# Optimization experiments

Hardware: AMD Instinct MI355X
Metric: run time of the kernel (lower is better)

The kernel has to match this reference:

```python
import jax, jax.numpy as jnp
import numpy as np

BETA = 0.25
LATENT_DIM = 256
CODEBOOK_DIM = 2048
CODE_DIM = 64


def setup_inputs() -> dict:
    key = jax.random.key(0)
    k_z, k_wi, k_bi, k_cb, k_wo, k_bo = jax.random.split(key, 6)
    z = jax.random.normal(k_z, (64, LATENT_DIM, 32, 32), dtype=jnp.float32)
    # project_in: Conv2d(latent_dim, code_dim, kernel_size=1) -> weight [code_dim, latent_dim]
    W_in = jax.random.normal(k_wi, (CODE_DIM, LATENT_DIM), dtype=jnp.float32) * (1.0 / np.sqrt(LATENT_DIM))
    b_in = jax.random.normal(k_bi, (CODE_DIM,), dtype=jnp.float32) * 0.01
    # codebook init: uniform(-1/codebook_dim, 1/codebook_dim) as in _codebook_init
    codebook = jax.random.uniform(k_cb, (CODEBOOK_DIM, CODE_DIM), dtype=jnp.float32,
                                  minval=-1.0 / CODEBOOK_DIM, maxval=1.0 / CODEBOOK_DIM)
    # project_out: Conv2d(code_dim, latent_dim, kernel_size=1) -> weight [latent_dim, code_dim]
    W_out = jax.random.normal(k_wo, (LATENT_DIM, CODE_DIM), dtype=jnp.float32) * (1.0 / np.sqrt(CODE_DIM))
    b_out = jax.random.normal(k_bo, (LATENT_DIM,), dtype=jnp.float32) * 0.01
    return {"z": z, "W_in": W_in, "b_in": b_in, "codebook": codebook, "W_out": W_out, "b_out": b_out}


def reference(z, W_in, b_in, codebook, W_out, b_out):
    sg = jax.lax.stop_gradient
    # project_in: 1x1 conv == per-pixel linear
    zp = jnp.einsum('bchw,dc->bdhw', z, W_in) + b_in[None, :, None, None]  # [b, code_dim, h, w]
    b, c, h, w = zp.shape
    ze = zp.transpose(0, 2, 3, 1).reshape(-1, c)  # [(b h w), code_dim]
    # euclidean distances: ||z||^2 - 2 z.W^T + ||W||^2
    dist = (jnp.sum(ze * ze, axis=1, keepdims=True)
            - 2.0 * ze @ codebook.T
            + jnp.sum(codebook * codebook, axis=1))  # [(b h w), codebook_dim]
    idx = jnp.argmin(dist, axis=1)  # [(b h w)]
    # decoder: embedding lookup
    zq = codebook[idx].reshape(b, h, w, c).transpose(0, 3, 1, 2)  # [b, code_dim, h, w]
    # VQ loss: codebook loss + beta * commitment loss
    codebook_loss = jnp.mean((zq - sg(zp)) ** 2)
    embedding_loss = jnp.mean((sg(zq) - zp) ** 2)
    loss = codebook_loss + BETA * embedding_loss
    # straight-through estimator
    zq_st = zp + sg(zq - zp)
    out = jnp.einsum('bchw,dc->bdhw', zq_st, W_out) + b_out[None, :, None, None]  # [b, latent_dim, h, w]
    return loss, out
```

## Files before the change

### kernel.cpp

```cpp
#include <hip/hip_runtime.h>
#include <hip/hip_bf16.h>

#define LATENT 256
#define CODED  64
#define NCODE  2048
#define HW     1024
#define KMASK  0xFFFFF800u

typedef __attribute__((ext_vector_type(8))) short  short8_t;
typedef __attribute__((ext_vector_type(4))) float  floatx4;

__device__ __forceinline__ unsigned int f2bf(float f){
    unsigned int x = __builtin_bit_cast(unsigned int, f);
    unsigned int r = (x + 0x7FFFu + ((x >> 16) & 1u)) >> 16;
    return r & 0xFFFFu;
}
__device__ __forceinline__ unsigned int pk2bf(float lo, float hi){
    return f2bf(lo) | (f2bf(hi) << 16);
}
__device__ __forceinline__ short8_t as_s8(uint4 u){ return __builtin_bit_cast(short8_t, u); }
__device__ __forceinline__ float    as_f (unsigned int u){ return __builtin_bit_cast(float, u); }
__device__ __forceinline__ unsigned int as_u(float f){ return __builtin_bit_cast(unsigned int, f); }

__global__ __launch_bounds__(256) void k_prep(const float* __restrict__ W_in,
        uint4* __restrict__ Wf, float* __restrict__ out0){
    int bid = blockIdx.x, tid = threadIdx.x;
    if (bid == 0 && tid == 0) out0[0] = 0.f;
    int chunk = bid*256 + tid;
    int lane = chunk & 63, kk = (chunk >> 6) & 7, t = chunk >> 9;
    int row = t*16 + (lane & 15), c0 = kk*32 + (lane >> 4)*8;
    const float* src = W_in + row*LATENT + c0;
    floatx4 f0 = *(const floatx4*)(src);
    floatx4 f1 = *(const floatx4*)(src + 4);
    uint4 o;
    o.x = pk2bf(f0[0], f0[1]); o.y = pk2bf(f0[2], f0[3]);
    o.z = pk2bf(f1[0], f1[1]); o.w = pk2bf(f1[2], f1[3]);
    Wf[chunk] = o;
}

__global__ __launch_bounds__(256) void k_projprep(const float* __restrict__ z,
        const uint4* __restrict__ Wf, const float* __restrict__ b_in,
        const float* __restrict__ cb, const float* __restrict__ W_out,
        const float* __restrict__ b_out, uint4* __restrict__ cbf,
        float* __restrict__ pcbT, uint4* __restrict__ keys4,
        uint4* __restrict__ zpf, float* __restrict__ out0){
    __shared__ __align__(16) unsigned int zpl[2048];
    __shared__ float ps[4];
    int bid = blockIdx.x, tid = threadIdx.x;
    if (bid < 64){
        int chunk = bid*256 + tid;
        int lane = chunk & 63, kk = (chunk >> 6) & 1, jt = chunk >> 7;
        int row = jt*16 + (lane & 15), c0 = kk*32 + (lane >> 4)*8;
        const float* src = cb + row*CODED + c0;
        floatx4 f0 = *(const floatx4*)(src);
        floatx4 f1 = *(const floatx4*)(src + 4);
        uint4 o;
        o.x = pk2bf(f0[0], f0[1]); o.y = pk2bf(f0[2], f0[3]);
        o.z = pk2bf(f1[0], f1[1]); o.w = pk2bf(f1[2], f1[3]);
        cbf[chunk] = o;
        return;
    }
    if (bid < 128){
        uint4 zz = {0u, 0u, 0u, 0u};
        keys4[(bid - 64)*256 + tid] = zz;
        return;
    }
    if (bid < 384){
        float* cbl = (float*)zpl;
        int j0 = (bid - 128)*8;
        for (int k = tid; k < 8*CODED; k += 256) cbl[k] = cb[j0*CODED + k];
        __syncthreads();
        float wrow[CODED];
        #pragma unroll
        for (int k = 0; k < 16; k++)
            ((floatx4*)wrow)[k] = ((const floatx4*)(W_out + tid*CODED))[k];
        float bo = b_out[tid];
        floatx4 lo, hi;
        #pragma unroll
        for (int jj = 0; jj < 8; jj++){
            float acc = bo;
            #pragma unroll
            for (int d = 0; d < CODED; d++) acc += cbl[jj*CODED + d]*wrow[d];
            if (jj < 4) lo[jj] = acc; else hi[jj-4] = acc;
        }
        *(floatx4*)(pcbT + (size_t)tid*NCODE + j0)     = lo;
        *(floatx4*)(pcbT + (size_t)tid*NCODE + j0 + 4) = hi;
        return;
    }
    int pbid = bid - 384;
    int wave = tid >> 6, lane = tid & 63;
    int col = lane & 15, g = lane >> 4;
    int b  = pbid >> 4;
    int p0 = (pbid & 15)*64;
    const unsigned int swz = (unsigned)((col & 7) << 2);

    floatx4 acc[4];
    #pragma unroll
    for (int t = 0; t < 4; t++) acc[t] = *(const floatx4*)(b_in + t*16 + g*4);
    const float* zp0 = z + ((size_t)b*LATENT + g*8)*HW + p0 + wave*16 + col;
    #pragma unroll 2
    for (int kk = 0; kk < 8; kk++){
        const float* zr = zp0 + (size_t)kk*32*HW;
        float f[8];
        #pragma unroll
        for (int i = 0; i < 8; i++) f[i] = zr[(size_t)i*HW];
        uint4 bu;
        bu.x = pk2bf(f[0], f[1]); bu.y = pk2bf(f[2], f[3]);
        bu.z = pk2bf(f[4], f[5]); bu.w = pk2bf(f[6], f[7]);
        short8_t bf = as_s8(bu);
        #pragma unroll
        for (int t = 0; t < 4; t++){
            short8_t af = as_s8(Wf[(t*8 + kk)*64 + lane]);
            acc[t] = __builtin_amdgcn_mfma_f32_16x16x32_bf16(af, bf, acc[t], 0, 0, 0);
        }
    }
    float s = 0.f;
    #pragma unroll
    for (int t = 0; t < 4; t++)
        #pragma unroll
        for (int r = 0; r < 4; r++) s += acc[t][r]*acc[t][r];
    #pragma unroll
    for (int off = 32; off; off >>= 1) s += __shfl_xor(s, off);
    if (lane == 0) ps[wave] = s;
    unsigned int* zb = zpl + (wave*16 + col)*32;
    #pragma unroll
    for (int t = 0; t < 4; t++){
        uint2 w;
        w.x = pk2bf(acc[t][0], acc[t][1]);
        w.y = pk2bf(acc[t][2], acc[t][3]);
        *(uint2*)(zb + (((unsigned)(t*8 + g*2)) ^ swz)) = w;
    }
    __syncthreads();
    int ptg = pbid*4 + wave;
    const unsigned int* zr = zpl + (wave*16 + col)*32;
    #pragma unroll
    for (int kk = 0; kk < 2; kk++){
        uint4 v = *(const uint4*)(zr + (((unsigned)(kk*16 + g*4)) ^ swz));
        zpf[(ptg*2 + kk)*64 + lane] = v;
    }
    if (tid == 0)
        atomicAdd(out0, (ps[0] + ps[1] + ps[2] + ps[3]) * (1.25f/4194304.f));
}

__global__ __launch_bounds__(256, 4) void k_argmin(const uint4* __restrict__ zpf,
        const uint4* __restrict__ cbf, unsigned int* __restrict__ keys){
    __shared__ uint4 atile[2][512];
    __shared__ float bestl[4][8][16];
    int tid = threadIdx.x, wave = tid >> 6, lane = tid & 63;
    int col = lane & 15, g = lane >> 4;
    int pxg = blockIdx.x & 511, jq = blockIdx.x >> 9;
    int pt0 = pxg*8;
    short8_t bfr[8][2];
    #pragma unroll
    for (int i = 0; i < 8; i++)
        #pragma unroll
        for (int kk = 0; kk < 2; kk++)
            bfr[i][kk] = as_s8(zpf[((pt0 + i)*2 + kk)*64 + lane]);
    const uint4* cbq = cbf + jq*4096;
    {   uint4 r0 = cbq[tid], r1 = cbq[256 + tid];
        atile[0][tid] = r0; atile[0][tid + 256] = r1; }
    __syncthreads();
    unsigned int jinv0 = 2047u - (unsigned)(jq*512 + wave*16 + g*4);
    unsigned int jinv1 = jinv0 - 1, jinv2 = jinv0 - 2, jinv3 = jinv0 - 3;
    float best[8];
    #pragma unroll
    for (int i = 0; i < 8; i++) best[i] = 0.f;
    const floatx4 ones = {1.f, 1.f, 1.f, 1.f};
    int cur = 0;
    for (int s = 0; s < 8; s++){
        uint4 r0, r1;
        if (s < 7){ r0 = cbq[(s+1)*512 + tid]; r1 = cbq[(s+1)*512 + 256 + tid]; }
        const uint4* ab = &atile[cur][wave*128];
        short8_t a0 = as_s8(ab[lane]);
        short8_t a1 = as_s8(ab[64 + lane]);
        #pragma unroll
        for (int i = 0; i < 8; i++){
            floatx4 d = __builtin_amdgcn_mfma_f32_16x16x32_bf16(a0, bfr[i][0], ones, 0, 0, 0);
            d = __builtin_amdgcn_mfma_f32_16x16x32_bf16(a1, bfr[i][1], d, 0, 0, 0);
            float k0 = as_f((as_u(d[0]) & KMASK) | jinv0);
            float k1 = as_f((as_u(d[1]) & KMASK) | jinv1);
            float k2 = as_f((as_u(d[2]) & KMASK) | jinv2);
            float k3 = as_f((as_u(d[3]) & KMASK) | jinv3);
            best[i] = fmaxf(best[i], fmaxf(fmaxf(k0, k1), fmaxf(k2, k3)));
        }
        jinv0 -= 64; jinv1 -= 64; jinv2 -= 64; jinv3 -= 64;
        if (s < 7){ atile[cur ^ 1][tid] = r0; atile[cur ^ 1][tid + 256] = r1; }
        __syncthreads();
        cur ^= 1;
    }
    #pragma unroll
    for (int i = 0; i < 8; i++){
        #pragma unroll
        for (int off = 16; off < 64; off <<= 1)
            best[i] = fmaxf(best[i], __shfl_xor(best[i], off));
    }
    if (lane < 16){
        #pragma unroll
        for (int i = 0; i < 8; i++) bestl[wave][i][lane] = best[i];
    }
    __syncthreads();
    if (lane < 16){
        #pragma unroll
        for (int q = 0; q < 2; q++){
            int i = wave*2 + q;
            float k = fmaxf(fmaxf(bestl[0][i][lane], bestl[1][i][lane]),
                            fmaxf(bestl[2][i][lane], bestl[3][i][lane]));
            atomicMax(&keys[(pt0 + i)*16 + lane], as_u(k));
        }
    }
}

__global__ __launch_bounds__(256) void k_out(const unsigned int* __restrict__ keys,
        const float* __restrict__ pcbT, float* __restrict__ outp,
        float* __restrict__ out0){
    __shared__ float rows[2*NCODE];
    __shared__ float ps2[4];
    int tid = threadIdx.x;
    int bg = blockIdx.x >> 7, nc = blockIdx.x & 127;
    int n0 = nc*2;
    #pragma unroll
    for (int q = 0; q < 2; q++){
        const floatx4* src = (const floatx4*)(pcbT + (size_t)(n0 + q)*NCODE);
        floatx4* dst = (floatx4*)(rows + q*NCODE);
        dst[tid]       = src[tid];
        dst[tid + 256] = src[tid + 256];
    }
    __syncthreads();
    float lp = 0.f;
    #pragma unroll
    for (int bb = 0; bb < 4; bb++){
        int b = bg*4 + bb;
        uint4 kv = *(const uint4*)(keys + b*HW + tid*4);
        int j0 = 2047 - (int)(kv.x & 0x7FFu);
        int j1 = 2047 - (int)(kv.y & 0x7FFu);
        int j2 = 2047 - (int)(kv.z & 0x7FFu);
        int j3 = 2047 - (int)(kv.w & 0x7FFu);
        float* ob = outp + ((size_t)b*LATENT + n0)*HW + tid*4;
        #pragma unroll
        for (int q = 0; q < 2; q++){
            const float* r = rows + q*NCODE;
            floatx4 v;
            v[0] = r[j0]; v[1] = r[j1]; v[2] = r[j2]; v[3] = r[j3];
            *(floatx4*)(ob + (size_t)q*HW) = v;
        }
        if (nc == 0)
            lp += 8.f - 2.f*(as_f(kv.x & KMASK) + as_f(kv.y & KMASK)
                           + as_f(kv.z & KMASK) + as_f(kv.w & KMASK));
    }
    if (nc == 0){
        #pragma unroll
        for (int o = 32; o; o >>= 1) lp += __shfl_down(lp, o);
        int wave = tid >> 6, lane = tid & 63;
        if (lane == 0) ps2[wave] = lp;
        __syncthreads();
        if (tid == 0)
            atomicAdd(out0, (ps2[0]+ps2[1]+ps2[2]+ps2[3]) * (1.25f/4194304.f));
    }
}

extern "C" void kernel_launch(void* const* d_in, const int* in_sizes, int n_in,
                              void* d_out, int out_size, void* d_ws, size_t ws_size,
                              hipStream_t stream) {
    (void)in_sizes; (void)n_in; (void)out_size; (void)ws_size;
    const float* z     = (const float*)d_in[0];
    const float* W_in  = (const float*)d_in[1];
    const float* b_in  = (const float*)d_in[2];
    const float* cb    = (const float*)d_in[3];
    const float* W_out = (const float*)d_in[4];
    const float* b_out = (const float*)d_in[5];
    float* outp = (float*)d_out;

    char* ws = (char*)d_ws;
    uint4*        cbf  = (uint4*)(ws);
    uint4*        Wf   = (uint4*)(ws + 262144);
    float*        pcbT = (float*)(ws + 294912);
    uint4*        zpf  = (uint4*)(ws + 2392064);
    unsigned int* keys = (unsigned int*)(ws + 10780672);

    k_prep    <<<8,    256, 0, stream>>>(W_in, Wf, outp);
    k_projprep<<<1408, 256, 0, stream>>>(z, Wf, b_in, cb, W_out, b_out,
                                         cbf, pcbT, (uint4*)keys, zpf, outp);
    k_argmin  <<<2048, 256, 0, stream>>>(zpf, cbf, keys);
    k_out     <<<2048, 256, 0, stream>>>(keys, pcbT, outp + 1, outp);
}
```

Measured before the change: 65.04 us.

## Fold W_in bf16 conversion into projection kernel and drop loss atomics

Removes the separate k_prep launch. Each projection block now converts W_in to bf16 fragments into shared memory itself, and the zeroing of the loss output moves into k_argmin. The per-block atomicAdd of the squared-norm loss term is replaced by writes of per-wave partials to a workspace, which k_out then sums in its reduction. This saves a kernel launch and atomic traffic, at the cost of 1024 blocks each redoing the W_in conversion (reading 64KB of W_in per block) and extra shared memory that may reduce occupancy.

After: 59.61 us. 8.4% less time.

```diff
diff --git a/kernel.cpp b/kernel.cpp
--- a/kernel.cpp
+++ b/kernel.cpp
@@ -22,30 +22,14 @@
 __device__ __forceinline__ float    as_f (unsigned int u){ return __builtin_bit_cast(float, u); }
 __device__ __forceinline__ unsigned int as_u(float f){ return __builtin_bit_cast(unsigned int, f); }
 
-__global__ __launch_bounds__(256) void k_prep(const float* __restrict__ W_in,
-        uint4* __restrict__ Wf, float* __restrict__ out0){
-    int bid = blockIdx.x, tid = threadIdx.x;
-    if (bid == 0 && tid == 0) out0[0] = 0.f;
-    int chunk = bid*256 + tid;
-    int lane = chunk & 63, kk = (chunk >> 6) & 7, t = chunk >> 9;
-    int row = t*16 + (lane & 15), c0 = kk*32 + (lane >> 4)*8;
-    const float* src = W_in + row*LATENT + c0;
-    floatx4 f0 = *(const floatx4*)(src);
-    floatx4 f1 = *(const floatx4*)(src + 4);
-    uint4 o;
-    o.x = pk2bf(f0[0], f0[1]); o.y = pk2bf(f0[2], f0[3]);
-    o.z = pk2bf(f1[0], f1[1]); o.w = pk2bf(f1[2], f1[3]);
-    Wf[chunk] = o;
-}
-
 __global__ __launch_bounds__(256) void k_projprep(const float* __restrict__ z,
-        const uint4* __restrict__ Wf, const float* __restrict__ b_in,
+        const float* __restrict__ W_in, const float* __restrict__ b_in,
         const float* __restrict__ cb, const float* __restrict__ W_out,
         const float* __restrict__ b_out, uint4* __restrict__ cbf,
         float* __restrict__ pcbT, uint4* __restrict__ keys4,
-        uint4* __restrict__ zpf, float* __restrict__ out0){
+        uint4* __restrict__ zpf, float* __restrict__ partials){
+    __shared__ __align__(16) uint4 wfl[2048];
     __shared__ __align__(16) unsigned int zpl[2048];
-    __shared__ float ps[4];
     int bid = blockIdx.x, tid = threadIdx.x;
     if (bid < 64){
         int chunk = bid*256 + tid;
@@ -94,6 +78,21 @@
     int p0 = (pbid & 15)*64;
     const unsigned int swz = (unsigned)((col & 7) << 2);
 
+    #pragma unroll
+    for (int k = 0; k < 8; k++){
+        int chunk = k*256 + tid;
+        int cl = chunk & 63, ckk = (chunk >> 6) & 7, ct = chunk >> 9;
+        int row = ct*16 + (cl & 15), c0 = ckk*32 + (cl >> 4)*8;
+        const float* src = W_in + row*LATENT + c0;
+        floatx4 f0 = *(const floatx4*)(src);
+        floatx4 f1 = *(const floatx4*)(src + 4);
+        uint4 o;
+        o.x = pk2bf(f0[0], f0[1]); o.y = pk2bf(f0[2], f0[3]);
+        o.z = pk2bf(f1[0], f1[1]); o.w = pk2bf(f1[2], f1[3]);
+        wfl[chunk] = o;
+    }
+    __syncthreads();
+
     floatx4 acc[4];
     #pragma unroll
     for (int t = 0; t < 4; t++) acc[t] = *(const floatx4*)(b_in + t*16 + g*4);
@@ -110,7 +109,7 @@
         short8_t bf = as_s8(bu);
         #pragma unroll
         for (int t = 0; t < 4; t++){
-            short8_t af = as_s8(Wf[(t*8 + kk)*64 + lane]);
+            short8_t af = as_s8(wfl[(t*8 + kk)*64 + lane]);
             acc[t] = __builtin_amdgcn_mfma_f32_16x16x32_bf16(af, bf, acc[t], 0, 0, 0);
         }
     }
@@ -121,7 +120,7 @@
         for (int r = 0; r < 4; r++) s += acc[t][r]*acc[t][r];
     #pragma unroll
     for (int off = 32; off; off >>= 1) s += __shfl_xor(s, off);
-    if (lane == 0) ps[wave] = s;
+    if (lane == 0) partials[pbid*4 + wave] = s;
     unsigned int* zb = zpl + (wave*16 + col)*32;
     #pragma unroll
     for (int t = 0; t < 4; t++){
@@ -132,22 +131,22 @@
     }
     __syncthreads();
     int ptg = pbid*4 + wave;
-    const unsigned int* zr = zpl + (wave*16 + col)*32;
+    const unsigned int* zr2 = zpl + (wave*16 + col)*32;
     #pragma unroll
     for (int kk = 0; kk < 2; kk++){
-        uint4 v = *(const uint4*)(zr + (((unsigned)(kk*16 + g*4)) ^ swz));
+        uint4 v = *(const uint4*)(zr2 + (((unsigned)(kk*16 + g*4)) ^ swz));
         zpf[(ptg*2 + kk)*64 + lane] = v;
     }
-    if (tid == 0)
-        atomicAdd(out0, (ps[0] + ps[1] + ps[2] + ps[3]) * (1.25f/4194304.f));
 }
 
 __global__ __launch_bounds__(256, 4) void k_argmin(const uint4* __restrict__ zpf,
-        const uint4* __restrict__ cbf, unsigned int* __restrict__ keys){
+        const uint4* __restrict__ cbf, unsigned int* __restrict__ keys,
+        float* __restrict__ out0){
     __shared__ uint4 atile[2][512];
     __shared__ float bestl[4][8][16];
     int tid = threadIdx.x, wave = tid >> 6, lane = tid & 63;
     int col = lane & 15, g = lane >> 4;
+    if (blockIdx.x == 0 && tid == 0) out0[0] = 0.f;
     int pxg = blockIdx.x & 511, jq = blockIdx.x >> 9;
     int pt0 = pxg*8;
     short8_t bfr[8][2];
@@ -211,8 +210,8 @@
 }
 
 __global__ __launch_bounds__(256) void k_out(const unsigned int* __restrict__ keys,
-        const float* __restrict__ pcbT, float* __restrict__ outp,
-        float* __restrict__ out0){
+        const float* __restrict__ pcbT, const float* __restrict__ partials,
+        float* __restrict__ outp, float* __restrict__ out0){
     __shared__ float rows[2*NCODE];
     __shared__ float ps2[4];
     int tid = threadIdx.x;
@@ -248,6 +247,7 @@
                            + as_f(kv.z & KMASK) + as_f(kv.w & KMASK));
     }
     if (nc == 0){
+        lp += partials[bg*256 + tid];
         #pragma unroll
         for (int o = 32; o; o >>= 1) lp += __shfl_down(lp, o);
         int wave = tid >> 6, lane = tid & 63;
@@ -271,15 +271,14 @@
     float* outp = (float*)d_out;
 
     char* ws = (char*)d_ws;
-    uint4*        cbf  = (uint4*)(ws);
-    uint4*        Wf   = (uint4*)(ws + 262144);
-    float*        pcbT = (float*)(ws + 294912);
-    uint4*        zpf  = (uint4*)(ws + 2392064);
-    unsigned int* keys = (unsigned int*)(ws + 10780672);
-
-    k_prep    <<<8,    256, 0, stream>>>(W_in, Wf, outp);
-    k_projprep<<<1408, 256, 0, stream>>>(z, Wf, b_in, cb, W_out, b_out,
-                                         cbf, pcbT, (uint4*)keys, zpf, outp);
-    k_argmin  <<<2048, 256, 0, stream>>>(zpf, cbf, keys);
-    k_out     <<<2048, 256, 0, stream>>>(keys, pcbT, outp + 1, outp);
-}
+    uint4*        cbf      = (uint4*)(ws);
+    float*        partials = (float*)(ws + 262144);
+    float*        pcbT     = (float*)(ws + 294912);
+    uint4*        zpf      = (uint4*)(ws + 2392064);
+    unsigned int* keys     = (unsigned int*)(ws + 10780672);
+
+    k_projprep<<<1408, 256, 0, stream>>>(z, W_in, b_in, cb, W_out, b_out,
+                                         cbf, pcbT, (uint4*)keys, zpf, partials);
+    k_argmin  <<<2048, 256, 0, stream>>>(zpf, cbf, keys, outp);
+    k_out     <<<2048, 256, 0, stream>>>(keys, pcbT, partials, outp + 1, outp);
+}
```
